# Optimization experiments

Measured on AMD Instinct MI355X. Metric: run time of the kernel, lower is better.

The kernel has to match this reference:

```python
import jax, jax.numpy as jnp
import numpy as np

VOCAB = 50000
D = 32            # hidden_size
OUT = 5           # output_size (sentiment classes)
B = 512           # number of balanced trees
L = 64            # leaves per tree (power of 2)


def setup_inputs() -> dict:
    key = jax.random.key(0)
    ks = jax.random.split(key, 6)
    # scale params down to avoid tanh saturation (original uses xavier init)
    return {
        "word_ids": jax.random.randint(ks[0], (B, L), 0, VOCAB, dtype=jnp.int32),
        "embed": jax.random.normal(ks[1], (VOCAB, D), jnp.float32) * 0.1,
        "V": jax.random.normal(ks[2], (D, 2 * D, 2 * D), jnp.float32) * 0.02,
        "W": jax.random.normal(ks[3], (2 * D, D), jnp.float32) * 0.1,
        "b": jnp.zeros((1, D), jnp.float32),
        "Wout_w": jax.random.normal(ks[4], (OUT, D), jnp.float32) * 0.1,
        "Wout_b": jnp.zeros((OUT,), jnp.float32),
    }


def reference(word_ids, embed, V, W, b, Wout_w, Wout_b):
    # Leaves: embedding lookup. h: [B, n_nodes_at_level, D]
    h = embed[word_ids]                              # [B, L, D]
    all_nodes = [h.reshape(-1, D)]
    n_levels = int(np.log2(h.shape[1]))
    for _ in range(n_levels):
        left = h[:, 0::2]                            # [B, n/2, D]
        right = h[:, 1::2]                           # [B, n/2, D]
        c = jnp.concatenate([left, right], axis=-1)  # [B, n/2, 2D]
        # xVx_k = c @ V_k @ c^T for each slice k of the tensor V
        Vc = jnp.einsum('kjl,bnl->bnkj', V, c)       # [B, n/2, D, 2D]
        xVx = jnp.einsum('bnj,bnkj->bnk', c, Vc)     # [B, n/2, D]
        h = jnp.tanh(xVx + c @ W + b)                # [B, n/2, D]
        all_nodes.append(h.reshape(-1, D))
    nodes = jnp.concatenate(all_nodes, axis=0)       # [B*(2L-1), D]
    logits = nodes @ Wout_w.T + Wout_b               # [B*(2L-1), OUT]
    log_probs = jax.nn.log_softmax(logits, axis=-1)
    roots = h[:, 0, :]                               # [B, D]
    return log_probs, roots
```

## Files before the change

### kernel.cpp

```cpp
#include <hip/hip_runtime.h>

#define OUT_N 5
#define TOTAL_NODES 65024
#define ROOTS_OFF (TOTAL_NODES * OUT_N)

typedef __attribute__((ext_vector_type(8))) short bf16x8;
typedef __attribute__((ext_vector_type(4))) float f32x4;
typedef __attribute__((ext_vector_type(8))) unsigned short ushort8v;
typedef __attribute__((ext_vector_type(4))) unsigned int uint4v;

static __device__ __forceinline__ unsigned short f2bf(float f) {
    union { float f; unsigned int i; } v; v.f = f;
    unsigned int r = v.i + 0x7fff + ((v.i >> 16) & 1);
    return (unsigned short)(r >> 16);
}

static __device__ __forceinline__ int naddr32(int R, int c) {
    return R * 128 + (((c + R) & 7) << 4);
}
static __device__ __forceinline__ void store_h32(char* smem, int R, int col, float v) {
    *(float*)(smem + naddr32(R, col >> 2) + (col & 3) * 4) = v;
}

__global__ __launch_bounds__(64) void bprep_kernel(
    const float* __restrict__ V, const float* __restrict__ W,
    unsigned short* __restrict__ B)
{
    int t = blockIdx.x * 64 + threadIdx.x;
    if (t >= 8576) return;
    int ks = t >> 7, sub = t & 127;
    int n = sub >> 6, lane = sub & 63;
    int hi = lane >> 4, l15 = lane & 15;
    int k = n * 16 + l15;
    const float* Vk = V + (size_t)k * 4096;
    ushort8v o;
    #pragma unroll
    for (int i = 0; i < 8; ++i) {
        int r5 = hi * 8 + i;
        float val;
        if (ks < 2)        { int j = 32 * ks + r5; val = Vk[j * 64 + j]; }
        else if (ks < 64)  { int d = ks >> 1; int j = 32 * (ks & 1) + r5; int l = (j + d) & 63;
                             val = Vk[j * 64 + l] + Vk[l * 64 + j]; }
        else if (ks == 64) { int j = r5; val = Vk[j * 64 + j + 32] + Vk[(j + 32) * 64 + j]; }
        else               { int j = (ks == 65) ? r5 : (32 + r5); val = W[j * 32 + k]; }
        o[i] = f2bf(val);
    }
    *(ushort8v*)(B + (size_t)t * 8) = o;
}

static __device__ __forceinline__ void load_crot32(
    const char* nodes, int Rc, int hi, float* crot)
{
    #pragma unroll
    for (int t = 0; t < 16; ++t) {
        int m = (hi * 2 + t) & 15;
        int row = Rc + (m >> 3), c4 = m & 7;
        f32x4 v = *(const f32x4*)(nodes + naddr32(row, c4));
        #pragma unroll
        for (int e = 0; e < 4; ++e) crot[t * 4 + e] = v[e];
    }
}

template<int K0, int K1>
static __device__ __forceinline__ void run2_k(
    const unsigned short* __restrict__ Bg, const float* crot,
    int lane, f32x4& a0, f32x4& a1)
{
    const char* bp = (const char*)Bg + lane * 16;
    #pragma unroll
    for (int ks = K0; ks < K1; ++ks) {
        uint4v aw;
        #pragma unroll
        for (int q = 0; q < 4; ++q) {
            int i0 = 2 * q, i1 = 2 * q + 1;
            float p0, p1;
            if (ks < 2)       { p0 = crot[32*ks+i0] * crot[32*ks+i0];
                                p1 = crot[32*ks+i1] * crot[32*ks+i1]; }
            else if (ks < 64) { const int bse = 32 * (ks & 1), d = ks >> 1;
                                p0 = crot[bse+i0] * crot[(bse+i0+d)&63];
                                p1 = crot[bse+i1] * crot[(bse+i1+d)&63]; }
            else if (ks == 64){ p0 = crot[i0] * crot[32+i0];
                                p1 = crot[i1] * crot[32+i1]; }
            else if (ks == 65){ p0 = crot[i0];    p1 = crot[i1]; }
            else              { p0 = crot[32+i0]; p1 = crot[32+i1]; }
            unsigned int pk;
            asm("v_cvt_pk_bf16_f32 %0, %1, %2" : "=v"(pk) : "v"(p0), "v"(p1));
            aw[q] = pk;
        }
        bf16x8 afr = __builtin_bit_cast(bf16x8, aw);
        bf16x8 b0 = *(const bf16x8*)(bp + (ks << 11));
        bf16x8 b1 = *(const bf16x8*)(bp + (ks << 11) + 1024);
        a0 = __builtin_amdgcn_mfma_f32_16x16x32_bf16(afr, b0, a0, 0, 0, 0);
        a1 = __builtin_amdgcn_mfma_f32_16x16x32_bf16(afr, b1, a1, 0, 0, 0);
    }
}

static __device__ __forceinline__ void node_logits32(
    const char* smem, int R, const float* __restrict__ Wout_w,
    const float* __restrict__ Wout_b, float* __restrict__ out, size_t g)
{
    float h[32];
    #pragma unroll
    for (int c = 0; c < 8; ++c) {
        f32x4 v = *(const f32x4*)(smem + naddr32(R, c));
        #pragma unroll
        for (int e = 0; e < 4; ++e) h[c * 4 + e] = v[e];
    }
    float lg[OUT_N];
    #pragma unroll
    for (int o = 0; o < OUT_N; ++o) {
        const float* w = Wout_w + o * 32;
        float s = 0.f;
        #pragma unroll
        for (int x = 0; x < 32; ++x) s = fmaf(w[x], h[x], s);
        lg[o] = s + Wout_b[o];
    }
    float m = lg[0];
    #pragma unroll
    for (int o = 1; o < OUT_N; ++o) m = fmaxf(m, lg[o]);
    float sum = 0.f;
    #pragma unroll
    for (int o = 0; o < OUT_N; ++o) sum += expf(lg[o] - m);
    float lse = m + logf(sum);
    #pragma unroll
    for (int o = 0; o < OUT_N; ++o) out[g * OUT_N + o] = lg[o] - lse;
}

__global__ __launch_bounds__(256, 4) void l1_kernel(
    const int* __restrict__ word_ids, const float* __restrict__ embed,
    const unsigned short* __restrict__ Bg, const float* __restrict__ bias,
    const float* __restrict__ Wout_w, const float* __restrict__ Wout_b,
    float* __restrict__ h1buf, float* __restrict__ out)
{
    __shared__ char smem[6144 + 6144];
    const int tid = threadIdx.x, lane = tid & 63;
    const int l15 = lane & 15, hi = lane >> 4, u = tid >> 6;
    const int tile = blockIdx.x;

    {
        int rr = tid >> 3, q4 = tid & 7;
        int r = rr >> 1, child = rr & 1;
        int g1 = tile * 16 + r;
        int leaf = (g1 >> 5) * 64 + (g1 & 31) * 2 + child;
        int wid = word_ids[leaf];
        f32x4 v = ((const f32x4*)(embed + (size_t)wid * 32))[q4];
        *(f32x4*)(smem + naddr32(rr, q4)) = v;

        float lg[OUT_N];
        #pragma unroll
        for (int o = 0; o < OUT_N; ++o) {
            const float* w = Wout_w + o * 32 + q4 * 4;
            lg[o] = w[0]*v[0] + w[1]*v[1] + w[2]*v[2] + w[3]*v[3];
        }
        #pragma unroll
        for (int o = 0; o < OUT_N; ++o) {
            lg[o] += __shfl_xor(lg[o], 1, 64);
            lg[o] += __shfl_xor(lg[o], 2, 64);
            lg[o] += __shfl_xor(lg[o], 4, 64);
        }
        if (q4 == 0) {
            #pragma unroll
            for (int o = 0; o < OUT_N; ++o) lg[o] += Wout_b[o];
            float m = lg[0];
            #pragma unroll
            for (int o = 1; o < OUT_N; ++o) m = fmaxf(m, lg[o]);
            float sum = 0.f;
            #pragma unroll
            for (int o = 0; o < OUT_N; ++o) sum += expf(lg[o] - m);
            float lse = m + logf(sum);
            #pragma unroll
            for (int o = 0; o < OUT_N; ++o) out[(size_t)leaf * OUT_N + o] = lg[o] - lse;
        }
    }
    __syncthreads();

    float crot[64];
    load_crot32(smem, 2 * l15, hi, crot);

    f32x4 a0 = {0.f,0.f,0.f,0.f}, a1 = {0.f,0.f,0.f,0.f};
    if      (u == 0) run2_k< 0, 17>(Bg, crot, lane, a0, a1);
    else if (u == 1) run2_k<17, 34>(Bg, crot, lane, a0, a1);
    else if (u == 2) run2_k<34, 50>(Bg, crot, lane, a0, a1);
    else             run2_k<50, 67>(Bg, crot, lane, a0, a1);

    if (u > 0) {
        char* sp = smem + 6144 + (u - 1) * 2048 + lane * 32;
        *(f32x4*)sp = a0; *((f32x4*)sp + 1) = a1;
    }
    __syncthreads();
    if (u == 0) {
        #pragma unroll
        for (int v2 = 0; v2 < 3; ++v2) {
            const char* sp = smem + 6144 + v2 * 2048 + lane * 32;
            a0 += *(const f32x4*)sp;
            a1 += *((const f32x4*)sp + 1);
        }
        float bk0 = bias[l15], bk1 = bias[16 + l15];
        #pragma unroll
        for (int r = 0; r < 4; ++r) {
            int row = hi * 4 + r;
            int node = tile * 16 + row;
            float h0 = tanhf(a0[r] + bk0), h1v = tanhf(a1[r] + bk1);
            h1buf[(size_t)node * 32 + l15]      = h0;
            h1buf[(size_t)node * 32 + 16 + l15] = h1v;
            store_h32(smem, 32 + row, l15, h0);
            store_h32(smem, 32 + row, 16 + l15, h1v);
        }
    }
    __syncthreads();
    if (tid < 16)
        node_logits32(smem, 32 + tid, Wout_w, Wout_b, out,
                      (size_t)32768 + tile * 16 + tid);
}

constexpr int SCR_T = 16384;

template<int RPT, int CHILDB, int OUTB, bool ROOT>
static __device__ __forceinline__ void level_deep(
    char* smem, const unsigned short* __restrict__ Bg,
    const float* __restrict__ bias, float* __restrict__ roots,
    int bid, int lane, int wave)
{
    const int l15 = lane & 15, hi = lane >> 4;
    int rc = (l15 < 2 * RPT) ? l15 : 0;
    int tree = rc / RPT, i = rc % RPT;
    float crot[64];
    load_crot32(smem, tree * 64 + CHILDB + 2 * i, hi, crot);

    f32x4 a0 = {0.f,0.f,0.f,0.f}, a1 = {0.f,0.f,0.f,0.f};
    switch (wave) {
        case 0:  run2_k< 0,  9>(Bg, crot, lane, a0, a1); break;
        case 1:  run2_k< 9, 17>(Bg, crot, lane, a0, a1); break;
        case 2:  run2_k<17, 26>(Bg, crot, lane, a0, a1); break;
        case 3:  run2_k<26, 34>(Bg, crot, lane, a0, a1); break;
        case 4:  run2_k<34, 42>(Bg, crot, lane, a0, a1); break;
        case 5:  run2_k<42, 50>(Bg, crot, lane, a0, a1); break;
        case 6:  run2_k<50, 59>(Bg, crot, lane, a0, a1); break;
        default: run2_k<59, 67>(Bg, crot, lane, a0, a1); break;
    }
    if (wave > 0) {
        char* sp = smem + SCR_T + (wave - 1) * 2048 + lane * 32;
        *(f32x4*)sp = a0; *((f32x4*)sp + 1) = a1;
    }
    __syncthreads();
    if (wave == 0) {
        #pragma unroll
        for (int v2 = 0; v2 < 7; ++v2) {
            const char* sp = smem + SCR_T + v2 * 2048 + lane * 32;
            a0 += *(const f32x4*)sp;
            a1 += *((const f32x4*)sp + 1);
        }
        float bk0 = bias[l15], bk1 = bias[16 + l15];
        #pragma unroll
        for (int r4 = 0; r4 < 4; ++r4) {
            int row = hi * 4 + r4;
            if (row < 2 * RPT) {
                float h0 = tanhf(a0[r4] + bk0), h1v = tanhf(a1[r4] + bk1);
                int t2 = row / RPT, i2 = row % RPT;
                int R2 = t2 * 64 + OUTB + i2;
                store_h32(smem, R2, l15, h0);
                store_h32(smem, R2, 16 + l15, h1v);
                if (ROOT) {
                    roots[(size_t)(bid * 2 + t2) * 32 + l15]      = h0;
                    roots[(size_t)(bid * 2 + t2) * 32 + 16 + l15] = h1v;
                }
            }
        }
    }
    __syncthreads();
}

__global__ __launch_bounds__(512, 2) void tail_kernel(
    const unsigned short* __restrict__ Bg, const float* __restrict__ bias,
    const float* __restrict__ h1buf,
    const float* __restrict__ Wout_w, const float* __restrict__ Wout_b,
    float* __restrict__ out)
{
    __shared__ char smem[16384 + 14336];
    const int tid = threadIdx.x, lane = tid & 63;
    const int l15 = lane & 15, hi = lane >> 4, wave = tid >> 6;
    const int bid = blockIdx.x;
    float* roots = out + ROOTS_OFF;

    {
        int gRow = tid >> 3, c4 = tid & 7;
        int t = gRow >> 5, i = gRow & 31;
        f32x4 v = *(const f32x4*)(h1buf + ((size_t)(bid * 2 + t) * 32 + i) * 32 + c4 * 4);
        *(f32x4*)(smem + naddr32(t * 64 + i, c4)) = v;
    }
    __syncthreads();

    {
        const int t = wave >> 2, u = wave & 3;
        float crot[64];
        load_crot32(smem, t * 64 + 2 * l15, hi, crot);
        f32x4 a0 = {0.f,0.f,0.f,0.f}, a1 = {0.f,0.f,0.f,0.f};
        if      (u == 0) run2_k< 0, 17>(Bg, crot, lane, a0, a1);
        else if (u == 1) run2_k<17, 34>(Bg, crot, lane, a0, a1);
        else if (u == 2) run2_k<34, 50>(Bg, crot, lane, a0, a1);
        else             run2_k<50, 67>(Bg, crot, lane, a0, a1);
        if (u > 0) {
            char* sp = smem + SCR_T + (t * 3 + u - 1) * 2048 + lane * 32;
            *(f32x4*)sp = a0; *((f32x4*)sp + 1) = a1;
        }
        __syncthreads();
        if (u == 0) {
            #pragma unroll
            for (int v2 = 0; v2 < 3; ++v2) {
                const char* sp = smem + SCR_T + (t * 3 + v2) * 2048 + lane * 32;
                a0 += *(const f32x4*)sp;
                a1 += *((const f32x4*)sp + 1);
            }
            float bk0 = bias[l15], bk1 = bias[16 + l15];
            #pragma unroll
            for (int r4 = 0; r4 < 4; ++r4) {
                int row = hi * 4 + r4;
                int R2 = t * 64 + 32 + row;
                float h0 = tanhf(a0[r4] + bk0), h1v = tanhf(a1[r4] + bk1);
                store_h32(smem, R2, l15, h0);
                store_h32(smem, R2, 16 + l15, h1v);
            }
        }
        __syncthreads();
    }

    level_deep<8, 32, 48, false>(smem, Bg, bias, roots, bid, lane, wave);
    level_deep<4, 48, 56, false>(smem, Bg, bias, roots, bid, lane, wave);
    level_deep<2, 56, 60, false>(smem, Bg, bias, roots, bid, lane, wave);
    level_deep<1, 60, 62, true >(smem, Bg, bias, roots, bid, lane, wave);

    if (tid < 62) {
        int t = (tid >= 31) ? 1 : 0;
        int rr = tid - 31 * t;
        int R; size_t g;
        int tg = bid * 2 + t;
        if (rr < 16)      { R = t*64 + 32 + rr;        g = 49152 + (size_t)tg*16 + rr; }
        else if (rr < 24) { R = t*64 + 48 + (rr-16);   g = 57344 + (size_t)tg*8  + (rr-16); }
        else if (rr < 28) { R = t*64 + 56 + (rr-24);   g = 61440 + (size_t)tg*4  + (rr-24); }
        else if (rr < 30) { R = t*64 + 60 + (rr-28);   g = 63488 + (size_t)tg*2  + (rr-28); }
        else              { R = t*64 + 62;             g = 64512 + (size_t)tg; }
        node_logits32(smem, R, Wout_w, Wout_b, out, g);
    }
}

extern "C" void kernel_launch(void* const* d_in, const int* in_sizes, int n_in,
                              void* d_out, int out_size, void* d_ws, size_t ws_size,
                              hipStream_t stream)
{
    const int*   word_ids = (const int*)  d_in[0];
    const float* embed    = (const float*)d_in[1];
    const float* V        = (const float*)d_in[2];
    const float* W        = (const float*)d_in[3];
    const float* bvec     = (const float*)d_in[4];
    const float* Wout_w   = (const float*)d_in[5];
    const float* Wout_b   = (const float*)d_in[6];
    float* out = (float*)d_out;

    unsigned short* Bfrag = (unsigned short*)d_ws;
    float* h1buf = (float*)((char*)d_ws + 137216);

    bprep_kernel<<<134, 64, 0, stream>>>(V, W, Bfrag);
    l1_kernel<<<1024, 256, 0, stream>>>(word_ids, embed, Bfrag, bvec,
                                        Wout_w, Wout_b, h1buf, out);
    tail_kernel<<<256, 512, 0, stream>>>(Bfrag, bvec, h1buf, Wout_w, Wout_b, out);
}
```

Before: 36.75 us.

## Fuse level-one and tail kernels into a single per-tree kernel

```diff
diff --git a/kernel.cpp b/kernel.cpp
--- a/kernel.cpp
+++ b/kernel.cpp
@@ -126,219 +126,125 @@
     for (int o = 0; o < OUT_N; ++o) out[g * OUT_N + o] = lg[o] - lse;
 }
 
-__global__ __launch_bounds__(256, 4) void l1_kernel(
+constexpr int SCR = 12288;
+
+template<int RPT, bool ROOT>
+static __device__ __forceinline__ void level_run(
+    char* smem, const unsigned short* __restrict__ Bg,
+    const float* __restrict__ bias, float* __restrict__ roots,
+    int bid, int lane, int u, int childb, int outb)
+{
+    const int l15 = lane & 15, hi = lane >> 4;
+    int rc = (RPT >= 16) ? l15 : ((l15 < RPT) ? l15 : 0);
+    float crot[64];
+    load_crot32(smem, childb + 2 * rc, hi, crot);
+
+    f32x4 a0 = {0.f,0.f,0.f,0.f}, a1 = {0.f,0.f,0.f,0.f};
+    switch (u) {
+        case 0:  run2_k< 0, 17>(Bg, crot, lane, a0, a1); break;
+        case 1:  run2_k<17, 34>(Bg, crot, lane, a0, a1); break;
+        case 2:  run2_k<34, 50>(Bg, crot, lane, a0, a1); break;
+        default: run2_k<50, 67>(Bg, crot, lane, a0, a1); break;
+    }
+    if (u > 0) {
+        char* sp = smem + SCR + (u - 1) * 2048 + lane * 32;
+        *(f32x4*)sp = a0; *((f32x4*)sp + 1) = a1;
+    }
+    __syncthreads();
+    if (u == 0) {
+        #pragma unroll
+        for (int v2 = 0; v2 < 3; ++v2) {
+            const char* sp = smem + SCR + v2 * 2048 + lane * 32;
+            a0 += *(const f32x4*)sp;
+            a1 += *((const f32x4*)sp + 1);
+        }
+        float bk0 = bias[l15], bk1 = bias[16 + l15];
+        #pragma unroll
+        for (int r4 = 0; r4 < 4; ++r4) {
+            int row = hi * 4 + r4;
+            if (row < RPT) {
+                float h0 = tanhf(a0[r4] + bk0), h1v = tanhf(a1[r4] + bk1);
+                store_h32(smem, outb + row, l15, h0);
+                store_h32(smem, outb + row, 16 + l15, h1v);
+                if (ROOT) {
+                    roots[(size_t)bid * 32 + l15]      = h0;
+                    roots[(size_t)bid * 32 + 16 + l15] = h1v;
+                }
+            }
+        }
+    }
+    __syncthreads();
+}
+
+__global__ __launch_bounds__(256, 4) void tree_kernel(
     const int* __restrict__ word_ids, const float* __restrict__ embed,
     const unsigned short* __restrict__ Bg, const float* __restrict__ bias,
     const float* __restrict__ Wout_w, const float* __restrict__ Wout_b,
-    float* __restrict__ h1buf, float* __restrict__ out)
-{
-    __shared__ char smem[6144 + 6144];
+    float* __restrict__ out)
+{
+    __shared__ char smem[12288 + 6144];
     const int tid = threadIdx.x, lane = tid & 63;
-    const int l15 = lane & 15, hi = lane >> 4, u = tid >> 6;
-    const int tile = blockIdx.x;
-
-    {
-        int rr = tid >> 3, q4 = tid & 7;
-        int r = rr >> 1, child = rr & 1;
-        int g1 = tile * 16 + r;
-        int leaf = (g1 >> 5) * 64 + (g1 & 31) * 2 + child;
-        int wid = word_ids[leaf];
-        f32x4 v = ((const f32x4*)(embed + (size_t)wid * 32))[q4];
-        *(f32x4*)(smem + naddr32(rr, q4)) = v;
-
-        float lg[OUT_N];
-        #pragma unroll
-        for (int o = 0; o < OUT_N; ++o) {
-            const float* w = Wout_w + o * 32 + q4 * 4;
-            lg[o] = w[0]*v[0] + w[1]*v[1] + w[2]*v[2] + w[3]*v[3];
-        }
-        #pragma unroll
-        for (int o = 0; o < OUT_N; ++o) {
-            lg[o] += __shfl_xor(lg[o], 1, 64);
-            lg[o] += __shfl_xor(lg[o], 2, 64);
-            lg[o] += __shfl_xor(lg[o], 4, 64);
-        }
-        if (q4 == 0) {
-            #pragma unroll
-            for (int o = 0; o < OUT_N; ++o) lg[o] += Wout_b[o];
-            float m = lg[0];
-            #pragma unroll
-            for (int o = 1; o < OUT_N; ++o) m = fmaxf(m, lg[o]);
-            float sum = 0.f;
-            #pragma unroll
-            for (int o = 0; o < OUT_N; ++o) sum += expf(lg[o] - m);
-            float lse = m + logf(sum);
-            #pragma unroll
-            for (int o = 0; o < OUT_N; ++o) out[(size_t)leaf * OUT_N + o] = lg[o] - lse;
-        }
-    }
-    __syncthreads();
-
-    float crot[64];
-    load_crot32(smem, 2 * l15, hi, crot);
-
-    f32x4 a0 = {0.f,0.f,0.f,0.f}, a1 = {0.f,0.f,0.f,0.f};
-    if      (u == 0) run2_k< 0, 17>(Bg, crot, lane, a0, a1);
-    else if (u == 1) run2_k<17, 34>(Bg, crot, lane, a0, a1);
-    else if (u == 2) run2_k<34, 50>(Bg, crot, lane, a0, a1);
-    else             run2_k<50, 67>(Bg, crot, lane, a0, a1);
-
-    if (u > 0) {
-        char* sp = smem + 6144 + (u - 1) * 2048 + lane * 32;
-        *(f32x4*)sp = a0; *((f32x4*)sp + 1) = a1;
-    }
-    __syncthreads();
-    if (u == 0) {
-        #pragma unroll
-        for (int v2 = 0; v2 < 3; ++v2) {
-            const char* sp = smem + 6144 + v2 * 2048 + lane * 32;
-            a0 += *(const f32x4*)sp;
-            a1 += *((const f32x4*)sp + 1);
-        }
-        float bk0 = bias[l15], bk1 = bias[16 + l15];
-        #pragma unroll
-        for (int r = 0; r < 4; ++r) {
-            int row = hi * 4 + r;
-            int node = tile * 16 + row;
-            float h0 = tanhf(a0[r] + bk0), h1v = tanhf(a1[r] + bk1);
-            h1buf[(size_t)node * 32 + l15]      = h0;
-            h1buf[(size_t)node * 32 + 16 + l15] = h1v;
-            store_h32(smem, 32 + row, l15, h0);
-            store_h32(smem, 32 + row, 16 + l15, h1v);
-        }
-    }
-    __syncthreads();
-    if (tid < 16)
-        node_logits32(smem, 32 + tid, Wout_w, Wout_b, out,
-                      (size_t)32768 + tile * 16 + tid);
-}
-
-constexpr int SCR_T = 16384;
-
-template<int RPT, int CHILDB, int OUTB, bool ROOT>
-static __device__ __forceinline__ void level_deep(
-    char* smem, const unsigned short* __restrict__ Bg,
-    const float* __restrict__ bias, float* __restrict__ roots,
-    int bid, int lane, int wave)
-{
-    const int l15 = lane & 15, hi = lane >> 4;
-    int rc = (l15 < 2 * RPT) ? l15 : 0;
-    int tree = rc / RPT, i = rc % RPT;
-    float crot[64];
-    load_crot32(smem, tree * 64 + CHILDB + 2 * i, hi, crot);
-
-    f32x4 a0 = {0.f,0.f,0.f,0.f}, a1 = {0.f,0.f,0.f,0.f};
-    switch (wave) {
-        case 0:  run2_k< 0,  9>(Bg, crot, lane, a0, a1); break;
-        case 1:  run2_k< 9, 17>(Bg, crot, lane, a0, a1); break;
-        case 2:  run2_k<17, 26>(Bg, crot, lane, a0, a1); break;
-        case 3:  run2_k<26, 34>(Bg, crot, lane, a0, a1); break;
-        case 4:  run2_k<34, 42>(Bg, crot, lane, a0, a1); break;
-        case 5:  run2_k<42, 50>(Bg, crot, lane, a0, a1); break;
-        case 6:  run2_k<50, 59>(Bg, crot, lane, a0, a1); break;
-        default: run2_k<59, 67>(Bg, crot, lane, a0, a1); break;
-    }
-    if (wave > 0) {
-        char* sp = smem + SCR_T + (wave - 1) * 2048 + lane * 32;
-        *(f32x4*)sp = a0; *((f32x4*)sp + 1) = a1;
-    }
-    __syncthreads();
-    if (wave == 0) {
-        #pragma unroll
-        for (int v2 = 0; v2 < 7; ++v2) {
-            const char* sp = smem + SCR_T + v2 * 2048 + lane * 32;
-            a0 += *(const f32x4*)sp;
-            a1 += *((const f32x4*)sp + 1);
-        }
-        float bk0 = bias[l15], bk1 = bias[16 + l15];
-        #pragma unroll
-        for (int r4 = 0; r4 < 4; ++r4) {
-            int row = hi * 4 + r4;
-            if (row < 2 * RPT) {
-                float h0 = tanhf(a0[r4] + bk0), h1v = tanhf(a1[r4] + bk1);
-                int t2 = row / RPT, i2 = row % RPT;
-                int R2 = t2 * 64 + OUTB + i2;
-                store_h32(smem, R2, l15, h0);
-                store_h32(smem, R2, 16 + l15, h1v);
-                if (ROOT) {
-                    roots[(size_t)(bid * 2 + t2) * 32 + l15]      = h0;
-                    roots[(size_t)(bid * 2 + t2) * 32 + 16 + l15] = h1v;
-                }
-            }
-        }
-    }
-    __syncthreads();
-}
-
-__global__ __launch_bounds__(512, 2) void tail_kernel(
-    const unsigned short* __restrict__ Bg, const float* __restrict__ bias,
-    const float* __restrict__ h1buf,
-    const float* __restrict__ Wout_w, const float* __restrict__ Wout_b,
-    float* __restrict__ out)
-{
-    __shared__ char smem[16384 + 14336];
-    const int tid = threadIdx.x, lane = tid & 63;
-    const int l15 = lane & 15, hi = lane >> 4, wave = tid >> 6;
+    const int u = tid >> 6;
     const int bid = blockIdx.x;
     float* roots = out + ROOTS_OFF;
 
-    {
-        int gRow = tid >> 3, c4 = tid & 7;
-        int t = gRow >> 5, i = gRow & 31;
-        f32x4 v = *(const f32x4*)(h1buf + ((size_t)(bid * 2 + t) * 32 + i) * 32 + c4 * 4);
-        *(f32x4*)(smem + naddr32(t * 64 + i, c4)) = v;
-    }
-    __syncthreads();
-
-    {
-        const int t = wave >> 2, u = wave & 3;
-        float crot[64];
-        load_crot32(smem, t * 64 + 2 * l15, hi, crot);
-        f32x4 a0 = {0.f,0.f,0.f,0.f}, a1 = {0.f,0.f,0.f,0.f};
-        if      (u == 0) run2_k< 0, 17>(Bg, crot, lane, a0, a1);
-        else if (u == 1) run2_k<17, 34>(Bg, crot, lane, a0, a1);
-        else if (u == 2) run2_k<34, 50>(Bg, crot, lane, a0, a1);
-        else             run2_k<50, 67>(Bg, crot, lane, a0, a1);
-        if (u > 0) {
-            char* sp = smem + SCR_T + (t * 3 + u - 1) * 2048 + lane * 32;
-            *(f32x4*)sp = a0; *((f32x4*)sp + 1) = a1;
+    #pragma unroll
+    for (int p = 0; p < 2; ++p) {
+        {
+            int rr = tid >> 3, q4 = tid & 7;
+            int leaf = (bid * 2 + p) * 32 + rr;
+            int wid = word_ids[leaf];
+            f32x4 v = ((const f32x4*)(embed + (size_t)wid * 32))[q4];
+            *(f32x4*)(smem + naddr32(64 + rr, q4)) = v;
+
+            float lg[OUT_N];
+            #pragma unroll
+            for (int o = 0; o < OUT_N; ++o) {
+                const float* w = Wout_w + o * 32 + q4 * 4;
+                lg[o] = w[0]*v[0] + w[1]*v[1] + w[2]*v[2] + w[3]*v[3];
+            }
+            #pragma unroll
+            for (int o = 0; o < OUT_N; ++o) {
+                lg[o] += __shfl_xor(lg[o], 1, 64);
+                lg[o] += __shfl_xor(lg[o], 2, 64);
+                lg[o] += __shfl_xor(lg[o], 4, 64);
+            }
+            if (q4 == 0) {
+                #pragma unroll
+                for (int o = 0; o < OUT_N; ++o) lg[o] += Wout_b[o];
+                float m = lg[0];
+                #pragma unroll
+                for (int o = 1; o < OUT_N; ++o) m = fmaxf(m, lg[o]);
+                float sum = 0.f;
+                #pragma unroll
+                for (int o = 0; o < OUT_N; ++o) sum += expf(lg[o] - m);
+                float lse = m + logf(sum);
+                #pragma unroll
+                for (int o = 0; o < OUT_N; ++o) out[(size_t)leaf * OUT_N + o] = lg[o] - lse;
+            }
         }
         __syncthreads();
-        if (u == 0) {
-            #pragma unroll
-            for (int v2 = 0; v2 < 3; ++v2) {
-                const char* sp = smem + SCR_T + (t * 3 + v2) * 2048 + lane * 32;
-                a0 += *(const f32x4*)sp;
-                a1 += *((const f32x4*)sp + 1);
-            }
-            float bk0 = bias[l15], bk1 = bias[16 + l15];
-            #pragma unroll
-            for (int r4 = 0; r4 < 4; ++r4) {
-                int row = hi * 4 + r4;
-                int R2 = t * 64 + 32 + row;
-                float h0 = tanhf(a0[r4] + bk0), h1v = tanhf(a1[r4] + bk1);
-                store_h32(smem, R2, l15, h0);
-                store_h32(smem, R2, 16 + l15, h1v);
-            }
-        }
-        __syncthreads();
-    }
-
-    level_deep<8, 32, 48, false>(smem, Bg, bias, roots, bid, lane, wave);
-    level_deep<4, 48, 56, false>(smem, Bg, bias, roots, bid, lane, wave);
-    level_deep<2, 56, 60, false>(smem, Bg, bias, roots, bid, lane, wave);
-    level_deep<1, 60, 62, true >(smem, Bg, bias, roots, bid, lane, wave);
-
-    if (tid < 62) {
-        int t = (tid >= 31) ? 1 : 0;
-        int rr = tid - 31 * t;
-        int R; size_t g;
-        int tg = bid * 2 + t;
-        if (rr < 16)      { R = t*64 + 32 + rr;        g = 49152 + (size_t)tg*16 + rr; }
-        else if (rr < 24) { R = t*64 + 48 + (rr-16);   g = 57344 + (size_t)tg*8  + (rr-16); }
-        else if (rr < 28) { R = t*64 + 56 + (rr-24);   g = 61440 + (size_t)tg*4  + (rr-24); }
-        else if (rr < 30) { R = t*64 + 60 + (rr-28);   g = 63488 + (size_t)tg*2  + (rr-28); }
-        else              { R = t*64 + 62;             g = 64512 + (size_t)tg; }
+        if (p == 0) level_run<16, false>(smem, Bg, bias, roots, bid, lane, u, 64, 0);
+        else        level_run<16, false>(smem, Bg, bias, roots, bid, lane, u, 64, 16);
+    }
+
+    if (tid < 32)
+        node_logits32(smem, tid, Wout_w, Wout_b, out,
+                      (size_t)32768 + (size_t)bid * 32 + tid);
+
+    level_run<16, false>(smem, Bg, bias, roots, bid, lane, u,  0, 32);
+    level_run< 8, false>(smem, Bg, bias, roots, bid, lane, u, 32, 48);
+    level_run< 4, false>(smem, Bg, bias, roots, bid, lane, u, 48, 56);
+    level_run< 2, false>(smem, Bg, bias, roots, bid, lane, u, 56, 60);
+    level_run< 1, true >(smem, Bg, bias, roots, bid, lane, u, 60, 62);
+
+    if (tid < 31) {
+        int rr = tid; int R; size_t g;
+        if (rr < 16)      { R = 32 + rr;        g = 49152 + (size_t)bid * 16 + rr; }
+        else if (rr < 24) { R = 48 + (rr - 16); g = 57344 + (size_t)bid * 8  + (rr - 16); }
+        else if (rr < 28) { R = 56 + (rr - 24); g = 61440 + (size_t)bid * 4  + (rr - 24); }
+        else if (rr < 30) { R = 60 + (rr - 28); g = 63488 + (size_t)bid * 2  + (rr - 28); }
+        else              { R = 62;             g = 64512 + (size_t)bid; }
         node_logits32(smem, R, Wout_w, Wout_b, out, g);
     }
 }
@@ -357,10 +263,8 @@
     float* out = (float*)d_out;
 
     unsigned short* Bfrag = (unsigned short*)d_ws;
-    float* h1buf = (float*)((char*)d_ws + 137216);
 
     bprep_kernel<<<134, 64, 0, stream>>>(V, W, Bfrag);
-    l1_kernel<<<1024, 256, 0, stream>>>(word_ids, embed, Bfrag, bvec,
-                                        Wout_w, Wout_b, h1buf, out);
-    tail_kernel<<<256, 512, 0, stream>>>(Bfrag, bvec, h1buf, Wout_w, Wout_b, out);
-}
+    tree_kernel<<<512, 256, 0, stream>>>(word_ids, embed, Bfrag, bvec,
+                                         Wout_w, Wout_b, out);
+}
```

After: 133.5 us. 3.63x slower.
